# Performance work log

Hardware: AMD Instinct MI355X
Metric: run time of the kernel (lower is better)

Reference implementation:

```python
import jax, jax.numpy as jnp
import numpy as np


def setup_inputs() -> dict:
    key = jax.random.key(0)
    kq, kk, kv = jax.random.split(key, 3)
    B, S, D = 4, 4096, 128
    q = jax.random.normal(kq, (B, S, D), dtype=jnp.float32)
    k = jax.random.normal(kk, (B, S, D), dtype=jnp.float32)
    v = jax.random.normal(kv, (B, S, D), dtype=jnp.float32)
    return {"q": q, "k": k, "v": v}


def reference(q, k, v):
    # naive scaled dot-product attention: softmax(q k^T / sqrt(d)) v
    scale = 1.0 / jnp.sqrt(jnp.asarray(q.shape[-1], q.dtype))
    scores = jnp.einsum("bsd,btd->bst", q, k) * scale  # [B,S,S]
    probs = jax.nn.softmax(scores, axis=-1)
    out = jnp.einsum("bst,btd->bsd", probs, v)  # [B,S,Dv]
    return out
```

## Files before the change

kernel.cpp:

```cpp
#include <hip/hip_runtime.h>
#include <cmath>
#include <cstdint>

typedef __attribute__((ext_vector_type(8))) __bf16 bf16x8;
typedef __attribute__((ext_vector_type(4))) float f32x4;
typedef unsigned int u32;
typedef unsigned short u16;

constexpr int Bn = 4, Sn = 4096, Dn = 128;
constexpr int OSTR = 132;
constexpr float SCL2E = 0.08838834764831845f * 1.4426950408889634f;

__device__ __forceinline__ u32 pk2(float a, float b) {
  u32 r;
  asm("v_cvt_pk_bf16_f32 %0, %1, %2" : "=v"(r) : "v"(a), "v"(b));
  return r;
}

__launch_bounds__(256)
__global__ void prep_kv(const float* __restrict__ Kg, const float* __restrict__ Vg,
                        u16* __restrict__ Kf, u16* __restrict__ Vf) {
  __shared__ float Tl[64 * 132];
  const int kt = blockIdx.x, b = blockIdx.y;
  const int tid = threadIdx.x;
  const size_t tileBase = ((size_t)b * 64 + kt) * 1024;

  #pragma unroll
  for (int r = 0; r < 8; ++r) {
    const int idx = tid + r * 256;
    const int row = idx >> 5, col = (idx & 31) * 4;
    float4 v = *(const float4*)(Kg + ((size_t)b * Sn + kt * 64 + row) * Dn + col);
    *(float4*)(Tl + row * 132 + col) = v;
  }
  __syncthreads();
  #pragma unroll
  for (int r = 0; r < 4; ++r) {
    const int g = tid + r * 256;
    const int l = g & 63, kt16 = (g >> 6) & 3, kc = g >> 8;
    const int row = kt16 * 16 + (l & 15), col = kc * 32 + (l >> 4) * 8;
    const float* s = Tl + row * 132 + col;
    float4 f0 = *(const float4*)(s);
    float4 f1 = *(const float4*)(s + 4);
    uint4 o;
    o.x = pk2(f0.x, f0.y); o.y = pk2(f0.z, f0.w);
    o.z = pk2(f1.x, f1.y); o.w = pk2(f1.z, f1.w);
    *(uint4*)(Kf + (tileBase + g) * 8) = o;
  }
  __syncthreads();

  #pragma unroll
  for (int r = 0; r < 8; ++r) {
    const int idx = tid + r * 256;
    const int row = idx >> 5, col = (idx & 31) * 4;
    float4 v = *(const float4*)(Vg + ((size_t)b * Sn + kt * 64 + row) * Dn + col);
    *(float4*)(Tl + row * 132 + col) = v;
  }
  __syncthreads();
  #pragma unroll
  for (int r = 0; r < 4; ++r) {
    const int g = tid + r * 256;
    const int l = g & 63, dt = (g >> 6) & 7, u = g >> 9;
    const int grp = l >> 4;
    const int col = dt * 16 + (l & 15);
    const int r0 = u * 32 + grp * 4;
    const int r1 = r0 + 16;
    float x[8];
    #pragma unroll
    for (int j = 0; j < 4; ++j) x[j] = Tl[(r0 + j) * 132 + col];
    #pragma unroll
    for (int j = 0; j < 4; ++j) x[4 + j] = Tl[(r1 + j) * 132 + col];
    uint4 o;
    o.x = pk2(x[0], x[1]); o.y = pk2(x[2], x[3]);
    o.z = pk2(x[4], x[5]); o.w = pk2(x[6], x[7]);
    *(uint4*)(Vf + (tileBase + g) * 8) = o;
  }
}

__launch_bounds__(256, 4)
__global__ void attn_mfma(const float* __restrict__ qg, const u16* __restrict__ Kf,
                          const u16* __restrict__ Vf, float* __restrict__ Og) {
  __shared__ __align__(16) unsigned char lds[34048];
  float* Oc = (float*)lds;
  float* ml = (float*)(lds + 33792);

  const int tid = threadIdx.x;
  const int kp = tid >> 6, lane = tid & 63;
  const int q = lane & 15, g = lane >> 4;
  const int b = blockIdx.x & 3;
  const int q0 = (blockIdx.x >> 2) * 16;

  const u16* Kb = Kf + ((size_t)b * 64) * 1024 * 8;
  const u16* Vb = Vf + ((size_t)b * 64) * 1024 * 8;

  bf16x8 qf[4];
  {
    const float* Qr = qg + ((size_t)b * Sn + q0 + q) * Dn + g * 8;
    #pragma unroll
    for (int kc = 0; kc < 4; ++kc) {
      float4 f0 = *(const float4*)(Qr + kc * 32);
      float4 f1 = *(const float4*)(Qr + kc * 32 + 4);
      uint4 t;
      t.x = pk2(f0.x * SCL2E, f0.y * SCL2E);
      t.y = pk2(f0.z * SCL2E, f0.w * SCL2E);
      t.z = pk2(f1.x * SCL2E, f1.y * SCL2E);
      t.w = pk2(f1.z * SCL2E, f1.w * SCL2E);
      qf[kc] = __builtin_bit_cast(bf16x8, t);
    }
  }

  f32x4 accO[8];
  #pragma unroll
  for (int dt = 0; dt < 8; ++dt)
    #pragma unroll
    for (int r = 0; r < 4; ++r) accO[dt][r] = 0.f;
  float l_i = 0.f;

  #pragma unroll 1
  for (int t8 = 0; t8 < 16; ++t8) {
    const int kt = kp * 16 + t8;
    const u16* Kt = Kb + (size_t)kt * 8192;
    const u16* Vt = Vb + (size_t)kt * 8192;

    f32x4 sa[4];
    #pragma unroll
    for (int t16 = 0; t16 < 4; ++t16)
      #pragma unroll
      for (int r = 0; r < 4; ++r) sa[t16][r] = 0.f;
    __builtin_amdgcn_s_setprio(1);
    #pragma unroll
    for (int kc = 0; kc < 4; ++kc) {
      #pragma unroll
      for (int t16 = 0; t16 < 4; ++t16) {
        uint4 a = *(const uint4*)(Kt + (size_t)((kc * 4 + t16) * 64 + lane) * 8);
        sa[t16] = __builtin_amdgcn_mfma_f32_16x16x32_bf16(
            __builtin_bit_cast(bf16x8, a), qf[kc], sa[t16], 0, 0, 0);
      }
    }
    __builtin_amdgcn_s_setprio(0);

    #pragma unroll
    for (int t16 = 0; t16 < 4; ++t16)
      #pragma unroll
      for (int r = 0; r < 4; ++r) { sa[t16][r] = exp2f(sa[t16][r]); l_i += sa[t16][r]; }

    __builtin_amdgcn_s_setprio(1);
    #pragma unroll
    for (int u = 0; u < 2; ++u) {
      uint4 pw;
      pw.x = pk2(sa[2 * u][0], sa[2 * u][1]);
      pw.y = pk2(sa[2 * u][2], sa[2 * u][3]);
      pw.z = pk2(sa[2 * u + 1][0], sa[2 * u + 1][1]);
      pw.w = pk2(sa[2 * u + 1][2], sa[2 * u + 1][3]);
      bf16x8 pf = __builtin_bit_cast(bf16x8, pw);
      #pragma unroll
      for (int dt = 0; dt < 8; ++dt) {
        uint4 av = *(const uint4*)(Vt + (size_t)((u * 8 + dt) * 64 + lane) * 8);
        accO[dt] = __builtin_amdgcn_mfma_f32_16x16x32_bf16(
            __builtin_bit_cast(bf16x8, av), pf, accO[dt], 0, 0, 0);
      }
    }
    __builtin_amdgcn_s_setprio(0);
  }

  l_i += __shfl_xor(l_i, 16);
  l_i += __shfl_xor(l_i, 32);

  {
    float* od = Oc + ((size_t)(kp * 16) + q) * OSTR + g * 4;
    #pragma unroll
    for (int dt = 0; dt < 8; ++dt) {
      float4 w = {accO[dt][0], accO[dt][1], accO[dt][2], accO[dt][3]};
      *(float4*)(od + dt * 16) = w;
    }
    if (lane < 16) ml[kp * 16 + q] = l_i;
  }
  __syncthreads();
  {
    const int row = tid >> 4;
    const int d0 = (tid & 15) * 8;
    float lsum = 0.f;
    #pragma unroll
    for (int k2 = 0; k2 < 4; ++k2) lsum += ml[k2 * 16 + row];
    const float inv = 1.f / lsum;
    float a[8] = {0.f, 0.f, 0.f, 0.f, 0.f, 0.f, 0.f, 0.f};
    #pragma unroll
    for (int k2 = 0; k2 < 4; ++k2) {
      const float* oc = Oc + (size_t)(k2 * 16 + row) * OSTR + d0;
      float4 v0 = *(const float4*)(oc);
      float4 v1 = *(const float4*)(oc + 4);
      a[0] += v0.x; a[1] += v0.y; a[2] += v0.z; a[3] += v0.w;
      a[4] += v1.x; a[5] += v1.y; a[6] += v1.z; a[7] += v1.w;
    }
    float* op = Og + ((size_t)b * Sn + q0 + row) * Dn + d0;
    float4 o0 = {a[0] * inv, a[1] * inv, a[2] * inv, a[3] * inv};
    float4 o1 = {a[4] * inv, a[5] * inv, a[6] * inv, a[7] * inv};
    *(float4*)(op) = o0;
    *(float4*)(op + 4) = o1;
  }
}

extern "C" void kernel_launch(void* const* d_in, const int* in_sizes, int n_in,
                              void* d_out, int out_size, void* d_ws, size_t ws_size,
                              hipStream_t stream) {
  const float* q = (const float*)d_in[0];
  const float* k = (const float*)d_in[1];
  const float* v = (const float*)d_in[2];
  float* out = (float*)d_out;
  const size_t N = (size_t)Bn * Sn * Dn;
  u16* Kf = (u16*)d_ws;
  u16* Vf = Kf + N;

  prep_kv<<<dim3(Sn / 64, Bn), dim3(256), 0, stream>>>(k, v, Kf, Vf);
  attn_mfma<<<dim3((Sn / 16) * Bn), dim3(256), 0, stream>>>(q, Kf, Vf, out);
}
```

Measured before the change: 143.4 us.

## Process 32 queries per block so each K/V fragment feeds two MFMAs

```diff
diff --git a/kernel.cpp b/kernel.cpp
--- a/kernel.cpp
+++ b/kernel.cpp
@@ -76,64 +76,73 @@
   }
 }
 
-__launch_bounds__(256, 4)
+__launch_bounds__(512)
 __global__ void attn_mfma(const float* __restrict__ qg, const u16* __restrict__ Kf,
                           const u16* __restrict__ Vf, float* __restrict__ Og) {
-  __shared__ __align__(16) unsigned char lds[34048];
+  __shared__ __align__(16) unsigned char lds[68608];
   float* Oc = (float*)lds;
-  float* ml = (float*)(lds + 33792);
+  float* ml = (float*)(lds + 67584);
 
   const int tid = threadIdx.x;
   const int kp = tid >> 6, lane = tid & 63;
   const int q = lane & 15, g = lane >> 4;
   const int b = blockIdx.x & 3;
-  const int q0 = (blockIdx.x >> 2) * 16;
+  const int q0 = (blockIdx.x >> 2) * 32;
 
   const u16* Kb = Kf + ((size_t)b * 64) * 1024 * 8;
   const u16* Vb = Vf + ((size_t)b * 64) * 1024 * 8;
 
-  bf16x8 qf[4];
+  bf16x8 qfA[4], qfB[4];
   {
-    const float* Qr = qg + ((size_t)b * Sn + q0 + q) * Dn + g * 8;
+    const float* QrA = qg + ((size_t)b * Sn + q0 + q) * Dn + g * 8;
+    const float* QrB = QrA + 16 * Dn;
     #pragma unroll
     for (int kc = 0; kc < 4; ++kc) {
-      float4 f0 = *(const float4*)(Qr + kc * 32);
-      float4 f1 = *(const float4*)(Qr + kc * 32 + 4);
-      uint4 t;
-      t.x = pk2(f0.x * SCL2E, f0.y * SCL2E);
-      t.y = pk2(f0.z * SCL2E, f0.w * SCL2E);
-      t.z = pk2(f1.x * SCL2E, f1.y * SCL2E);
-      t.w = pk2(f1.z * SCL2E, f1.w * SCL2E);
-      qf[kc] = __builtin_bit_cast(bf16x8, t);
-    }
-  }
-
-  f32x4 accO[8];
+      float4 a0 = *(const float4*)(QrA + kc * 32);
+      float4 a1 = *(const float4*)(QrA + kc * 32 + 4);
+      float4 b0 = *(const float4*)(QrB + kc * 32);
+      float4 b1 = *(const float4*)(QrB + kc * 32 + 4);
+      uint4 ta, tb;
+      ta.x = pk2(a0.x * SCL2E, a0.y * SCL2E);
+      ta.y = pk2(a0.z * SCL2E, a0.w * SCL2E);
+      ta.z = pk2(a1.x * SCL2E, a1.y * SCL2E);
+      ta.w = pk2(a1.z * SCL2E, a1.w * SCL2E);
+      tb.x = pk2(b0.x * SCL2E, b0.y * SCL2E);
+      tb.y = pk2(b0.z * SCL2E, b0.w * SCL2E);
+      tb.z = pk2(b1.x * SCL2E, b1.y * SCL2E);
+      tb.w = pk2(b1.z * SCL2E, b1.w * SCL2E);
+      qfA[kc] = __builtin_bit_cast(bf16x8, ta);
+      qfB[kc] = __builtin_bit_cast(bf16x8, tb);
+    }
+  }
+
+  f32x4 accA[8], accB[8];
   #pragma unroll
   for (int dt = 0; dt < 8; ++dt)
     #pragma unroll
-    for (int r = 0; r < 4; ++r) accO[dt][r] = 0.f;
-  float l_i = 0.f;
+    for (int r = 0; r < 4; ++r) { accA[dt][r] = 0.f; accB[dt][r] = 0.f; }
+  float lA = 0.f, lB = 0.f;
 
   #pragma unroll 1
-  for (int t8 = 0; t8 < 16; ++t8) {
-    const int kt = kp * 16 + t8;
+  for (int t8 = 0; t8 < 8; ++t8) {
+    const int kt = kp * 8 + t8;
     const u16* Kt = Kb + (size_t)kt * 8192;
     const u16* Vt = Vb + (size_t)kt * 8192;
 
-    f32x4 sa[4];
+    f32x4 saA[4], saB[4];
     #pragma unroll
     for (int t16 = 0; t16 < 4; ++t16)
       #pragma unroll
-      for (int r = 0; r < 4; ++r) sa[t16][r] = 0.f;
+      for (int r = 0; r < 4; ++r) { saA[t16][r] = 0.f; saB[t16][r] = 0.f; }
     __builtin_amdgcn_s_setprio(1);
     #pragma unroll
     for (int kc = 0; kc < 4; ++kc) {
       #pragma unroll
       for (int t16 = 0; t16 < 4; ++t16) {
         uint4 a = *(const uint4*)(Kt + (size_t)((kc * 4 + t16) * 64 + lane) * 8);
-        sa[t16] = __builtin_amdgcn_mfma_f32_16x16x32_bf16(
-            __builtin_bit_cast(bf16x8, a), qf[kc], sa[t16], 0, 0, 0);
+        bf16x8 af = __builtin_bit_cast(bf16x8, a);
+        saA[t16] = __builtin_amdgcn_mfma_f32_16x16x32_bf16(af, qfA[kc], saA[t16], 0, 0, 0);
+        saB[t16] = __builtin_amdgcn_mfma_f32_16x16x32_bf16(af, qfB[kc], saB[t16], 0, 0, 0);
       }
     }
     __builtin_amdgcn_s_setprio(0);
@@ -141,38 +150,66 @@
     #pragma unroll
     for (int t16 = 0; t16 < 4; ++t16)
       #pragma unroll
-      for (int r = 0; r < 4; ++r) { sa[t16][r] = exp2f(sa[t16][r]); l_i += sa[t16][r]; }
+      for (int r = 0; r < 4; ++r) {
+        saA[t16][r] = exp2f(saA[t16][r]); lA += saA[t16][r];
+        saB[t16][r] = exp2f(saB[t16][r]); lB += saB[t16][r];
+      }
 
     __builtin_amdgcn_s_setprio(1);
     #pragma unroll
     for (int u = 0; u < 2; ++u) {
-      uint4 pw;
-      pw.x = pk2(sa[2 * u][0], sa[2 * u][1]);
-      pw.y = pk2(sa[2 * u][2], sa[2 * u][3]);
-      pw.z = pk2(sa[2 * u + 1][0], sa[2 * u + 1][1]);
-      pw.w = pk2(sa[2 * u + 1][2], sa[2 * u + 1][3]);
-      bf16x8 pf = __builtin_bit_cast(bf16x8, pw);
+      uint4 pwA, pwB;
+      pwA.x = pk2(saA[2 * u][0], saA[2 * u][1]);
+      pwA.y = pk2(saA[2 * u][2], saA[2 * u][3]);
+      pwA.z = pk2(saA[2 * u + 1][0], saA[2 * u + 1][1]);
+      pwA.w = pk2(saA[2 * u + 1][2], saA[2 * u + 1][3]);
+      pwB.x = pk2(saB[2 * u][0], saB[2 * u][1]);
+      pwB.y = pk2(saB[2 * u][2], saB[2 * u][3]);
+      pwB.z = pk2(saB[2 * u + 1][0], saB[2 * u + 1][1]);
+      pwB.w = pk2(saB[2 * u + 1][2], saB[2 * u + 1][3]);
+      bf16x8 pfA = __builtin_bit_cast(bf16x8, pwA);
+      bf16x8 pfB = __builtin_bit_cast(bf16x8, pwB);
       #pragma unroll
       for (int dt = 0; dt < 8; ++dt) {
         uint4 av = *(const uint4*)(Vt + (size_t)((u * 8 + dt) * 64 + lane) * 8);
-        accO[dt] = __builtin_amdgcn_mfma_f32_16x16x32_bf16(
-            __builtin_bit_cast(bf16x8, av), pf, accO[dt], 0, 0, 0);
+        bf16x8 vf = __builtin_bit_cast(bf16x8, av);
+        accA[dt] = __builtin_amdgcn_mfma_f32_16x16x32_bf16(vf, pfA, accA[dt], 0, 0, 0);
+        accB[dt] = __builtin_amdgcn_mfma_f32_16x16x32_bf16(vf, pfB, accB[dt], 0, 0, 0);
       }
     }
     __builtin_amdgcn_s_setprio(0);
   }
 
-  l_i += __shfl_xor(l_i, 16);
-  l_i += __shfl_xor(l_i, 32);
+  lA += __shfl_xor(lA, 16); lA += __shfl_xor(lA, 32);
+  lB += __shfl_xor(lB, 16); lB += __shfl_xor(lB, 32);
 
   {
-    float* od = Oc + ((size_t)(kp * 16) + q) * OSTR + g * 4;
-    #pragma unroll
-    for (int dt = 0; dt < 8; ++dt) {
-      float4 w = {accO[dt][0], accO[dt][1], accO[dt][2], accO[dt][3]};
-      *(float4*)(od + dt * 16) = w;
-    }
-    if (lane < 16) ml[kp * 16 + q] = l_i;
+    float* odA = Oc + ((size_t)((kp & 3) * 32) + q) * OSTR + g * 4;
+    float* odB = odA + 16 * OSTR;
+    if (kp >= 4) {
+      #pragma unroll
+      for (int dt = 0; dt < 8; ++dt) {
+        float4 wa = {accA[dt][0], accA[dt][1], accA[dt][2], accA[dt][3]};
+        float4 wb = {accB[dt][0], accB[dt][1], accB[dt][2], accB[dt][3]};
+        *(float4*)(odA + dt * 16) = wa;
+        *(float4*)(odB + dt * 16) = wb;
+      }
+    }
+    if (lane < 16) { ml[kp * 32 + q] = lA; ml[kp * 32 + 16 + q] = lB; }
+    __syncthreads();
+    if (kp < 4) {
+      #pragma unroll
+      for (int dt = 0; dt < 8; ++dt) {
+        float4 pa = *(const float4*)(odA + dt * 16);
+        float4 pb = *(const float4*)(odB + dt * 16);
+        float4 wa = {accA[dt][0] + pa.x, accA[dt][1] + pa.y,
+                     accA[dt][2] + pa.z, accA[dt][3] + pa.w};
+        float4 wb = {accB[dt][0] + pb.x, accB[dt][1] + pb.y,
+                     accB[dt][2] + pb.z, accB[dt][3] + pb.w};
+        *(float4*)(odA + dt * 16) = wa;
+        *(float4*)(odB + dt * 16) = wb;
+      }
+    }
   }
   __syncthreads();
   {
@@ -180,12 +217,12 @@
     const int d0 = (tid & 15) * 8;
     float lsum = 0.f;
     #pragma unroll
-    for (int k2 = 0; k2 < 4; ++k2) lsum += ml[k2 * 16 + row];
+    for (int k2 = 0; k2 < 8; ++k2) lsum += ml[k2 * 32 + row];
     const float inv = 1.f / lsum;
     float a[8] = {0.f, 0.f, 0.f, 0.f, 0.f, 0.f, 0.f, 0.f};
     #pragma unroll
     for (int k2 = 0; k2 < 4; ++k2) {
-      const float* oc = Oc + (size_t)(k2 * 16 + row) * OSTR + d0;
+      const float* oc = Oc + (size_t)(k2 * 32 + row) * OSTR + d0;
       float4 v0 = *(const float4*)(oc);
       float4 v1 = *(const float4*)(oc + 4);
       a[0] += v0.x; a[1] += v0.y; a[2] += v0.z; a[3] += v0.w;
@@ -211,5 +248,5 @@
   u16* Vf = Kf + N;
 
   prep_kv<<<dim3(Sn / 64, Bn), dim3(256), 0, stream>>>(k, v, Kf, Vf);
-  attn_mfma<<<dim3((Sn / 16) * Bn), dim3(256), 0, stream>>>(q, Kf, Vf, out);
-}
+  attn_mfma<<<dim3((Sn / 32) * Bn), dim3(512), 0, stream>>>(q, Kf, Vf, out);
+}
```

Result: no change. 141.3 us (-1.4%).
